# Kernel optimization log

Measured on AMD Instinct MI355X. Metric: run time of the kernel, lower is better.

Reference implementation:

```python
import jax, jax.numpy as jnp
import numpy as np

SR = 44100.0
BLOCK = 128
FC_MIN, FC_MAX = 2000.0, 20000.0
Q_MIN, Q_MAX = 0.1, 10.0


def setup_inputs() -> dict:
    key = jax.random.key(0)
    k1, k2 = jax.random.split(key)
    x = jax.random.normal(k1, (32, 1, 262144), dtype=jnp.float32)
    control_params = jax.random.uniform(k2, (32, 2, 262144), dtype=jnp.float32)
    return {"x": x, "control_params": control_params}


def _lowpass(x, control_params):
    B, _, S = x.shape
    nb = S // BLOCK  # S is a multiple of BLOCK, so no padding branch needed
    # AvgPool1d(kernel_size=BLOCK): one control value per block
    cp = control_params.reshape(B, 2, nb, BLOCK).mean(axis=-1)  # (B, 2, nb)
    # denormalize_parameters: linear map from [0,1] into (min, max)
    fc = cp[:, 0] * (FC_MAX - FC_MIN) + FC_MIN  # (B, nb)
    q = cp[:, 1] * (Q_MAX - Q_MIN) + Q_MIN      # (B, nb)
    # RBJ cookbook low-pass biquad coefficients, normalized by a0
    w0 = 2.0 * jnp.pi * fc / SR
    alpha = jnp.sin(w0) / (2.0 * q)
    cosw = jnp.cos(w0)
    a0 = 1.0 + alpha
    b0 = ((1.0 - cosw) * 0.5) / a0
    b1 = (1.0 - cosw) / a0
    b2 = b0
    a1 = (-2.0 * cosw) / a0
    a2 = (1.0 - alpha) / a0
    # Each block is filtered independently with zero initial state
    # (the torch loop calls sosfilt fresh per block) -> vectorize over B*nb lanes.
    xb = x.reshape(B, nb, BLOCK).reshape(B * nb, BLOCK)
    b0f, b1f, b2f = b0.reshape(-1), b1.reshape(-1), b2.reshape(-1)
    a1f, a2f = a1.reshape(-1), a2.reshape(-1)
    xt = xb.T  # (BLOCK, B*nb): scan over time within a block

    def step(carry, xn):
        # direct form II transposed biquad
        z1, z2 = carry
        y = b0f * xn + z1
        z1n = b1f * xn - a1f * y + z2
        z2n = b2f * xn - a2f * y
        return (z1n, z2n), y

    zeros = jnp.zeros((B * nb,), dtype=x.dtype)
    _, ys = jax.lax.scan(step, (zeros, zeros), xt)  # ys: (BLOCK, B*nb)
    out = ys.T.reshape(B, nb, BLOCK).reshape(B, 1, S)
    return out, fc, q


def reference(x, control_params):
    # returns (output, cutoff_freq_per_block, q_factor_per_block)
    return _lowpass(x, control_params)
```

## Files before the change

### kernel.cpp

```cpp
#include <hip/hip_runtime.h>
#include <math.h>

constexpr int   BATCH = 32;
constexpr int   S     = 262144;
constexpr int   BLK   = 128;
constexpr int   NB    = S / BLK;
constexpr float SRATE = 44100.0f;
constexpr float FC_MIN = 2000.0f, FC_MAX = 20000.0f;
constexpr float Q_MIN  = 0.1f,    Q_MAX  = 10.0f;

__global__ __launch_bounds__(256) void lowpass_kernel(
    const float* __restrict__ x,
    const float* __restrict__ cp,
    float* __restrict__ out,
    float* __restrict__ fc_out,
    float* __restrict__ q_out)
{
    const int tid = blockIdx.x * blockDim.x + threadIdx.x;
    const int b   = tid >> 11;
    const int blk = tid & (NB - 1);

    const float4* c0 = reinterpret_cast<const float4*>(
        cp + (size_t)b * 2 * S + (size_t)blk * BLK);
    const float4* c1 = c0 + S / 4;

    float s0 = 0.0f, s1 = 0.0f;
#pragma unroll 8
    for (int j = 0; j < BLK / 4; ++j) {
        float4 v = c0[j];
        s0 += (v.x + v.y) + (v.z + v.w);
    }
#pragma unroll 8
    for (int j = 0; j < BLK / 4; ++j) {
        float4 v = c1[j];
        s1 += (v.x + v.y) + (v.z + v.w);
    }
    const float m0 = s0 * (1.0f / BLK);
    const float m1 = s1 * (1.0f / BLK);

    const float fc = m0 * (FC_MAX - FC_MIN) + FC_MIN;
    const float q  = m1 * (Q_MAX - Q_MIN) + Q_MIN;

    const float w0 = 6.283185307179586f * fc / SRATE;
    float sw, cw;
    sincosf(w0, &sw, &cw);
    const float alpha = sw / (2.0f * q);
    const float a0inv = 1.0f / (1.0f + alpha);
    const float b0c = (1.0f - cw) * 0.5f * a0inv;
    const float b1c = (1.0f - cw) * a0inv;
    const float a1c = (-2.0f * cw) * a0inv;
    const float a2c = (1.0f - alpha) * a0inv;

    const float4* xp = reinterpret_cast<const float4*>(
        x + (size_t)b * S + (size_t)blk * BLK);
    float4* op = reinterpret_cast<float4*>(
        out + (size_t)b * S + (size_t)blk * BLK);

    float z1 = 0.0f, z2 = 0.0f;
#pragma unroll 8
    for (int j = 0; j < BLK / 4; ++j) {
        float4 xv = xp[j];
        float4 yv;

        {   float xn = xv.x;
            float y  = b0c * xn + z1;
            float z1n = b1c * xn - a1c * y + z2;
            z2 = b0c * xn - a2c * y;
            z1 = z1n;
            yv.x = y; }
        {   float xn = xv.y;
            float y  = b0c * xn + z1;
            float z1n = b1c * xn - a1c * y + z2;
            z2 = b0c * xn - a2c * y;
            z1 = z1n;
            yv.y = y; }
        {   float xn = xv.z;
            float y  = b0c * xn + z1;
            float z1n = b1c * xn - a1c * y + z2;
            z2 = b0c * xn - a2c * y;
            z1 = z1n;
            yv.z = y; }
        {   float xn = xv.w;
            float y  = b0c * xn + z1;
            float z1n = b1c * xn - a1c * y + z2;
            z2 = b0c * xn - a2c * y;
            z1 = z1n;
            yv.w = y; }

        op[j] = yv;
    }

    fc_out[tid] = fc;
    q_out[tid]  = q;
}

extern "C" void kernel_launch(void* const* d_in, const int* in_sizes, int n_in,
                              void* d_out, int out_size, void* d_ws, size_t ws_size,
                              hipStream_t stream) {
    const float* x  = (const float*)d_in[0];
    const float* cp = (const float*)d_in[1];

    float* out    = (float*)d_out;
    float* fc_out = out + (size_t)BATCH * S;
    float* q_out  = fc_out + (size_t)BATCH * NB;

    const int total = BATCH * NB;
    lowpass_kernel<<<total / 256, 256, 0, stream>>>(x, cp, out, fc_out, q_out);
}
```

Baseline: 29.83 us.

## Stage x tiles through LDS with coalesced loads and cooperative control averaging

```diff
diff --git a/kernel.cpp b/kernel.cpp
--- a/kernel.cpp
+++ b/kernel.cpp
@@ -9,89 +9,129 @@
 constexpr float FC_MIN = 2000.0f, FC_MAX = 20000.0f;
 constexpr float Q_MIN  = 0.1f,    Q_MAX  = 10.0f;
 
-__global__ __launch_bounds__(256) void lowpass_kernel(
+constexpr int WPB     = 64;
+constexpr int THREADS = 256;
+
+
+__global__ __launch_bounds__(THREADS) void lowpass_kernel(
     const float* __restrict__ x,
     const float* __restrict__ cp,
     float* __restrict__ out,
     float* __restrict__ fc_out,
     float* __restrict__ q_out)
 {
-    const int tid = blockIdx.x * blockDim.x + threadIdx.x;
-    const int b   = tid >> 11;
-    const int blk = tid & (NB - 1);
+    __shared__ float xs[WPB * BLK];
+    __shared__ float ms0[WPB], ms1[WPB];
 
-    const float4* c0 = reinterpret_cast<const float4*>(
-        cp + (size_t)b * 2 * S + (size_t)blk * BLK);
-    const float4* c1 = c0 + S / 4;
+    const int t    = threadIdx.x;
+    const int wg   = blockIdx.x;
+    const int b    = wg >> 5;
+    const int blk0 = (wg & 31) * WPB;
 
-    float s0 = 0.0f, s1 = 0.0f;
-#pragma unroll 8
-    for (int j = 0; j < BLK / 4; ++j) {
-        float4 v = c0[j];
-        s0 += (v.x + v.y) + (v.z + v.w);
-    }
-#pragma unroll 8
-    for (int j = 0; j < BLK / 4; ++j) {
-        float4 v = c1[j];
-        s1 += (v.x + v.y) + (v.z + v.w);
-    }
-    const float m0 = s0 * (1.0f / BLK);
-    const float m1 = s1 * (1.0f / BLK);
+    const size_t xbase = (size_t)b * S + (size_t)blk0 * BLK;
+    const float4* x4 = reinterpret_cast<const float4*>(x + xbase);
 
-    const float fc = m0 * (FC_MAX - FC_MIN) + FC_MIN;
-    const float q  = m1 * (Q_MAX - Q_MIN) + Q_MIN;
-
-    const float w0 = 6.283185307179586f * fc / SRATE;
-    float sw, cw;
-    sincosf(w0, &sw, &cw);
-    const float alpha = sw / (2.0f * q);
-    const float a0inv = 1.0f / (1.0f + alpha);
-    const float b0c = (1.0f - cw) * 0.5f * a0inv;
-    const float b1c = (1.0f - cw) * a0inv;
-    const float a1c = (-2.0f * cw) * a0inv;
-    const float a2c = (1.0f - alpha) * a0inv;
-
-    const float4* xp = reinterpret_cast<const float4*>(
-        x + (size_t)b * S + (size_t)blk * BLK);
-    float4* op = reinterpret_cast<float4*>(
-        out + (size_t)b * S + (size_t)blk * BLK);
-
-    float z1 = 0.0f, z2 = 0.0f;
-#pragma unroll 8
-    for (int j = 0; j < BLK / 4; ++j) {
-        float4 xv = xp[j];
-        float4 yv;
-
-        {   float xn = xv.x;
-            float y  = b0c * xn + z1;
-            float z1n = b1c * xn - a1c * y + z2;
-            z2 = b0c * xn - a2c * y;
-            z1 = z1n;
-            yv.x = y; }
-        {   float xn = xv.y;
-            float y  = b0c * xn + z1;
-            float z1n = b1c * xn - a1c * y + z2;
-            z2 = b0c * xn - a2c * y;
-            z1 = z1n;
-            yv.y = y; }
-        {   float xn = xv.z;
-            float y  = b0c * xn + z1;
-            float z1n = b1c * xn - a1c * y + z2;
-            z2 = b0c * xn - a2c * y;
-            z1 = z1n;
-            yv.z = y; }
-        {   float xn = xv.w;
-            float y  = b0c * xn + z1;
-            float z1n = b1c * xn - a1c * y + z2;
-            z2 = b0c * xn - a2c * y;
-            z1 = z1n;
-            yv.w = y; }
-
-        op[j] = yv;
+#pragma unroll
+    for (int k = 0; k < 8; ++k) {
+        const int D  = k * THREADS + t;
+        const int B  = D >> 5;
+        const int jp = D & 31;
+        const int src4 = B * 32 + (jp ^ (B & 7));
+        float* ldsb = xs + (size_t)(k * THREADS + (t & ~63)) * 4;
+        __builtin_amdgcn_global_load_lds(
+            (const __attribute__((address_space(1))) void*)(x4 + src4),
+            (__attribute__((address_space(3))) void*)ldsb,
+            16, 0, 0);
     }
 
-    fc_out[tid] = fc;
-    q_out[tid]  = q;
+    const size_t cpb = (size_t)b * 2 * S + (size_t)blk0 * BLK;
+    const float4* c0 = reinterpret_cast<const float4*>(cp + cpb);
+    const float4* c1 = reinterpret_cast<const float4*>(cp + cpb + S);
+
+    float4 v0[8], v1[8];
+#pragma unroll
+    for (int k = 0; k < 8; ++k) {
+        const int f = k * THREADS + t;
+        v0[k] = c0[f];
+        v1[k] = c1[f];
+    }
+#pragma unroll
+    for (int k = 0; k < 8; ++k) {
+        float s0 = (v0[k].x + v0[k].y) + (v0[k].z + v0[k].w);
+        float s1 = (v1[k].x + v1[k].y) + (v1[k].z + v1[k].w);
+#pragma unroll
+        for (int m = 1; m < 32; m <<= 1) {
+            s0 += __shfl_xor(s0, m);
+            s1 += __shfl_xor(s1, m);
+        }
+        if ((t & 31) == 0) {
+            const int B = k * 8 + (t >> 5);
+            ms0[B] = s0;
+            ms1[B] = s1;
+        }
+    }
+
+    __syncthreads();
+
+    if (t < WPB) {
+        const float m0 = ms0[t] * (1.0f / BLK);
+        const float m1 = ms1[t] * (1.0f / BLK);
+        const float fc = m0 * (FC_MAX - FC_MIN) + FC_MIN;
+        const float q  = m1 * (Q_MAX - Q_MIN) + Q_MIN;
+
+        const int gblk = b * NB + blk0 + t;
+        fc_out[gblk] = fc;
+        q_out[gblk]  = q;
+
+        const float w0 = 6.283185307179586f * fc / SRATE;
+        float sw, cw;
+        sincosf(w0, &sw, &cw);
+        const float alpha = sw / (2.0f * q);
+        const float a0inv = 1.0f / (1.0f + alpha);
+        const float b0c = (1.0f - cw) * 0.5f * a0inv;
+        const float b1c = (1.0f - cw) * a0inv;
+        const float a1c = (-2.0f * cw) * a0inv;
+        const float a2c = (1.0f - alpha) * a0inv;
+
+        float4* xs4 = reinterpret_cast<float4*>(xs);
+        const int swz = t & 7;
+        float z1 = 0.0f, z2 = 0.0f;
+#pragma unroll 8
+        for (int j = 0; j < 32; ++j) {
+            const int a = t * 32 + (j ^ swz);
+            float4 xv = xs4[a];
+            float4 yv;
+            {   float xn = xv.x;
+                float y   = b0c * xn + z1;
+                float z1n = b1c * xn - a1c * y + z2;
+                z2 = b0c * xn - a2c * y;  z1 = z1n;  yv.x = y; }
+            {   float xn = xv.y;
+                float y   = b0c * xn + z1;
+                float z1n = b1c * xn - a1c * y + z2;
+                z2 = b0c * xn - a2c * y;  z1 = z1n;  yv.y = y; }
+            {   float xn = xv.z;
+                float y   = b0c * xn + z1;
+                float z1n = b1c * xn - a1c * y + z2;
+                z2 = b0c * xn - a2c * y;  z1 = z1n;  yv.z = y; }
+            {   float xn = xv.w;
+                float y   = b0c * xn + z1;
+                float z1n = b1c * xn - a1c * y + z2;
+                z2 = b0c * xn - a2c * y;  z1 = z1n;  yv.w = y; }
+            xs4[a] = yv;
+        }
+    }
+
+    __syncthreads();
+
+    float4* o4 = reinterpret_cast<float4*>(out + xbase);
+    const float4* xs4 = reinterpret_cast<const float4*>(xs);
+#pragma unroll
+    for (int k = 0; k < 8; ++k) {
+        const int D  = k * THREADS + t;
+        const int B  = D >> 5;
+        const int jp = D & 31;
+        o4[B * 32 + (jp ^ (B & 7))] = xs4[D];
+    }
 }
 
 extern "C" void kernel_launch(void* const* d_in, const int* in_sizes, int n_in,
@@ -104,6 +144,7 @@
     float* fc_out = out + (size_t)BATCH * S;
     float* q_out  = fc_out + (size_t)BATCH * NB;
 
-    const int total = BATCH * NB;
-    lowpass_kernel<<<total / 256, 256, 0, stream>>>(x, cp, out, fc_out, q_out);
+    const int total_blocks = BATCH * NB;
+    const int grid = total_blocks / WPB;
+    lowpass_kernel<<<grid, THREADS, 0, stream>>>(x, cp, out, fc_out, q_out);
 }
```

Measured after the change: 27.72 us. -7.1%, faster.

## Stage x through swizzled LDS with async loads and cooperative coalesced control averaging

Applied to the files above, without the earlier changes.

```diff
diff --git a/kernel.cpp b/kernel.cpp
--- a/kernel.cpp
+++ b/kernel.cpp
@@ -9,89 +9,142 @@
 constexpr float FC_MIN = 2000.0f, FC_MAX = 20000.0f;
 constexpr float Q_MIN  = 0.1f,    Q_MAX  = 10.0f;
 
-__global__ __launch_bounds__(256) void lowpass_kernel(
+constexpr int WPB     = 32;
+constexpr int TILES   = 2;
+constexpr int THREADS = 256;
+constexpr int T_X4    = WPB * BLK / 4;
+
+typedef float f32x4 __attribute__((ext_vector_type(4)));
+
+#define GLOAD(dst, p)                                                     \
+  asm volatile("global_load_dwordx4 %0, %1, off"                          \
+               : "=v"(dst) : "v"(p) : "memory")
+
+#define PROCESS(U, VMSTR, R0, R1)                                          \
+  do {                                                                     \
+    asm volatile("s_waitcnt vmcnt(" VMSTR ")"                              \
+                 : "+v"(R0[0]), "+v"(R0[1]), "+v"(R0[2]), "+v"(R0[3]),     \
+                   "+v"(R1[0]), "+v"(R1[1]), "+v"(R1[2]), "+v"(R1[3]));    \
+    _Pragma("unroll")                                                      \
+    for (int k = 0; k < 4; ++k) {                                          \
+      float s0 = (R0[k].x + R0[k].y) + (R0[k].z + R0[k].w);                \
+      float s1 = (R1[k].x + R1[k].y) + (R1[k].z + R1[k].w);                \
+      s0 += __shfl_xor(s0, 1);  s1 += __shfl_xor(s1, 1);                   \
+      s0 += __shfl_xor(s0, 2);  s1 += __shfl_xor(s1, 2);                   \
+      s0 += __shfl_xor(s0, 4);  s1 += __shfl_xor(s1, 4);                   \
+      s0 += __shfl_xor(s0, 8);  s1 += __shfl_xor(s1, 8);                   \
+      s0 += __shfl_xor(s0, 16); s1 += __shfl_xor(s1, 16);                  \
+      if ((t & 31) == 0) {                                                 \
+        const int Bseg = k * 8 + (t >> 5);                                 \
+        ms0[U][Bseg] = s0;                                                 \
+        ms1[U][Bseg] = s1;                                                 \
+      }                                                                    \
+    }                                                                      \
+    asm volatile("s_waitcnt lgkmcnt(0)\n\ts_barrier" ::: "memory");        \
+    if (t < WPB) {                                                         \
+      const float m0 = ms0[U][t] * (1.0f / BLK);                           \
+      const float m1 = ms1[U][t] * (1.0f / BLK);                           \
+      const float fcv = m0 * (FC_MAX - FC_MIN) + FC_MIN;                   \
+      const float qv  = m1 * (Q_MAX - Q_MIN) + Q_MIN;                      \
+      const int gblk = b * NB + blk0 + (U) * WPB + t;                      \
+      fc_out[gblk] = fcv;                                                  \
+      q_out[gblk]  = qv;                                                   \
+      const float w0 = 6.283185307179586f * fcv / SRATE;                   \
+      float sw, cw;                                                        \
+      sincosf(w0, &sw, &cw);                                               \
+      const float alpha = sw / (2.0f * qv);                                \
+      const float a0inv = 1.0f / (1.0f + alpha);                           \
+      const float b0c = (1.0f - cw) * 0.5f * a0inv;          \
+      const float b1c = (1.0f - cw) * a0inv;                               \
+      const float a1c = (-2.0f * cw) * a0inv;                              \
+      const float a2c = (1.0f - alpha) * a0inv;                            \
+      f32x4* xs4u = reinterpret_cast<f32x4*>(xs[U]);                       \
+      const int swz = t & 7;                                               \
+      float z1 = 0.0f, z2 = 0.0f;                                          \
+      _Pragma("unroll 8")                                                  \
+      for (int j = 0; j < 32; ++j) {                                       \
+        const int a = t * 32 + (j ^ swz);                                  \
+        f32x4 xv = xs4u[a];                                                \
+        f32x4 yv;                                                          \
+        { float xn = xv.x; float y = b0c * xn + z1;                        \
+          float z1n = b1c * xn - a1c * y + z2;                             \
+          z2 = b0c * xn - a2c * y; z1 = z1n; yv.x = y; }                   \
+        { float xn = xv.y; float y = b0c * xn + z1;                        \
+          float z1n = b1c * xn - a1c * y + z2;                             \
+          z2 = b0c * xn - a2c * y; z1 = z1n; yv.y = y; }                   \
+        { float xn = xv.z; float y = b0c * xn + z1;                        \
+          float z1n = b1c * xn - a1c * y + z2;                             \
+          z2 = b0c * xn - a2c * y; z1 = z1n; yv.z = y; }                   \
+        { float xn = xv.w; float y = b0c * xn + z1;                        \
+          float z1n = b1c * xn - a1c * y + z2;                             \
+          z2 = b0c * xn - a2c * y; z1 = z1n; yv.w = y; }                   \
+        xs4u[a] = yv;                \
+      }                                                                    \
+    }                                                                      \
+    asm volatile("s_waitcnt lgkmcnt(0)\n\ts_barrier" ::: "memory");        \
+    {                                                                      \
+      f32x4* o4 = reinterpret_cast<f32x4*>(out + xbase);                   \
+      const f32x4* xs4u = reinterpret_cast<const f32x4*>(xs[U]);           \
+      _Pragma("unroll")                                                    \
+      for (int k = 0; k < 4; ++k) {                                        \
+        const int D  = k * THREADS + t;                                    \
+        const int Br = D >> 5;                                             \
+        const int jp = D & 31;                                             \
+        o4[(U) * T_X4 + Br * 32 + (jp ^ (Br & 7))] = xs4u[D];              \
+      }                                                                    \
+    }                                                                      \
+  } while (0)
+
+__global__ __launch_bounds__(THREADS) void lowpass_kernel(
     const float* __restrict__ x,
     const float* __restrict__ cp,
     float* __restrict__ out,
     float* __restrict__ fc_out,
     float* __restrict__ q_out)
 {
-    const int tid = blockIdx.x * blockDim.x + threadIdx.x;
-    const int b   = tid >> 11;
-    const int blk = tid & (NB - 1);
+    __shared__ float xs[TILES][WPB * BLK];
+    __shared__ float ms0[TILES][WPB], ms1[TILES][WPB];
 
-    const float4* c0 = reinterpret_cast<const float4*>(
-        cp + (size_t)b * 2 * S + (size_t)blk * BLK);
-    const float4* c1 = c0 + S / 4;
+    const int t    = threadIdx.x;
+    const int wg   = blockIdx.x;
+    const int b    = wg >> 5;
+    const int blk0 = (wg & 31) * (WPB * TILES);
 
-    float s0 = 0.0f, s1 = 0.0f;
-#pragma unroll 8
-    for (int j = 0; j < BLK / 4; ++j) {
-        float4 v = c0[j];
-        s0 += (v.x + v.y) + (v.z + v.w);
+    const size_t xbase = (size_t)b * S + (size_t)blk0 * BLK;
+    const f32x4* x4 = reinterpret_cast<const f32x4*>(x + xbase);
+    const f32x4* c0 = reinterpret_cast<const f32x4*>(
+        cp + (size_t)b * 2 * S + (size_t)blk0 * BLK);
+    const f32x4* c1 = c0 + S / 4;
+
+    f32x4 c0a[4], c1a[4], c0b[4], c1b[4];
+
+#pragma unroll
+    for (int k = 0; k < 4; ++k) {
+        const int D = k * THREADS + t, B = D >> 5, jp = D & 31;
+        __builtin_amdgcn_global_load_lds(
+            (const __attribute__((address_space(1))) void*)(x4 + (B * 32 + (jp ^ (B & 7)))),
+            (__attribute__((address_space(3))) void*)(&xs[0][(k * THREADS + (t & ~63)) * 4]),
+            16, 0, 0);
     }
-#pragma unroll 8
-    for (int j = 0; j < BLK / 4; ++j) {
-        float4 v = c1[j];
-        s1 += (v.x + v.y) + (v.z + v.w);
+#pragma unroll
+    for (int k = 0; k < 4; ++k) GLOAD(c0a[k], c0 + k * THREADS + t);
+#pragma unroll
+    for (int k = 0; k < 4; ++k) GLOAD(c1a[k], c1 + k * THREADS + t);
+#pragma unroll
+    for (int k = 0; k < 4; ++k) {
+        const int D = k * THREADS + t, B = D >> 5, jp = D & 31;
+        __builtin_amdgcn_global_load_lds(
+            (const __attribute__((address_space(1))) void*)(x4 + (T_X4 + B * 32 + (jp ^ (B & 7)))),
+            (__attribute__((address_space(3))) void*)(&xs[1][(k * THREADS + (t & ~63)) * 4]),
+            16, 0, 0);
     }
-    const float m0 = s0 * (1.0f / BLK);
-    const float m1 = s1 * (1.0f / BLK);
+#pragma unroll
+    for (int k = 0; k < 4; ++k) GLOAD(c0b[k], c0 + T_X4 + k * THREADS + t);
+#pragma unroll
+    for (int k = 0; k < 4; ++k) GLOAD(c1b[k], c1 + T_X4 + k * THREADS + t);
 
-    const float fc = m0 * (FC_MAX - FC_MIN) + FC_MIN;
-    const float q  = m1 * (Q_MAX - Q_MIN) + Q_MIN;
-
-    const float w0 = 6.283185307179586f * fc / SRATE;
-    float sw, cw;
-    sincosf(w0, &sw, &cw);
-    const float alpha = sw / (2.0f * q);
-    const float a0inv = 1.0f / (1.0f + alpha);
-    const float b0c = (1.0f - cw) * 0.5f * a0inv;
-    const float b1c = (1.0f - cw) * a0inv;
-    const float a1c = (-2.0f * cw) * a0inv;
-    const float a2c = (1.0f - alpha) * a0inv;
-
-    const float4* xp = reinterpret_cast<const float4*>(
-        x + (size_t)b * S + (size_t)blk * BLK);
-    float4* op = reinterpret_cast<float4*>(
-        out + (size_t)b * S + (size_t)blk * BLK);
-
-    float z1 = 0.0f, z2 = 0.0f;
-#pragma unroll 8
-    for (int j = 0; j < BLK / 4; ++j) {
-        float4 xv = xp[j];
-        float4 yv;
-
-        {   float xn = xv.x;
-            float y  = b0c * xn + z1;
-            float z1n = b1c * xn - a1c * y + z2;
-            z2 = b0c * xn - a2c * y;
-            z1 = z1n;
-            yv.x = y; }
-        {   float xn = xv.y;
-            float y  = b0c * xn + z1;
-            float z1n = b1c * xn - a1c * y + z2;
-            z2 = b0c * xn - a2c * y;
-            z1 = z1n;
-            yv.y = y; }
-        {   float xn = xv.z;
-            float y  = b0c * xn + z1;
-            float z1n = b1c * xn - a1c * y + z2;
-            z2 = b0c * xn - a2c * y;
-            z1 = z1n;
-            yv.z = y; }
-        {   float xn = xv.w;
-            float y  = b0c * xn + z1;
-            float z1n = b1c * xn - a1c * y + z2;
-            z2 = b0c * xn - a2c * y;
-            z1 = z1n;
-            yv.w = y; }
-
-        op[j] = yv;
-    }
-
-    fc_out[tid] = fc;
-    q_out[tid]  = q;
+    PROCESS(0, "12", c0a, c1a);
+    PROCESS(1, "4", c0b, c1b);
 }
 
 extern "C" void kernel_launch(void* const* d_in, const int* in_sizes, int n_in,
@@ -104,6 +157,7 @@
     float* fc_out = out + (size_t)BATCH * S;
     float* q_out  = fc_out + (size_t)BATCH * NB;
 
-    const int total = BATCH * NB;
-    lowpass_kernel<<<total / 256, 256, 0, stream>>>(x, cp, out, fc_out, q_out);
+    const int total_blocks = BATCH * NB;
+    const int grid = total_blocks / (WPB * TILES);
+    lowpass_kernel<<<grid, THREADS, 0, stream>>>(x, cp, out, fc_out, q_out);
 }
```

After: 30.89 us. 1.04x slower.

## Parallelize each block's biquad recurrence across 32 lanes with a matrix-power scan

Applied to the files above, without the earlier changes.

```diff
diff --git a/kernel.cpp b/kernel.cpp
--- a/kernel.cpp
+++ b/kernel.cpp
@@ -9,37 +9,44 @@
 constexpr float FC_MIN = 2000.0f, FC_MAX = 20000.0f;
 constexpr float Q_MIN  = 0.1f,    Q_MAX  = 10.0f;
 
-__global__ __launch_bounds__(256) void lowpass_kernel(
-    const float* __restrict__ x,
-    const float* __restrict__ cp,
-    float* __restrict__ out,
+
+__global__ __launch_bounds__(256) void lowpass_scan_kernel(
+    const float4* __restrict__ x4,
+    const float4* __restrict__ cp4,
+    float4* __restrict__ o4,
     float* __restrict__ fc_out,
     float* __restrict__ q_out)
 {
-    const int tid = blockIdx.x * blockDim.x + threadIdx.x;
-    const int b   = tid >> 11;
-    const int blk = tid & (NB - 1);
+    const int tid  = blockIdx.x * blockDim.x + threadIdx.x;
+    const int lane = tid & 63;
+    const int r    = lane & 31;
+    const int blkg = tid >> 5;
+    const int b    = blkg >> 11;
+    const int blkL = blkg & (NB - 1);
 
-    const float4* c0 = reinterpret_cast<const float4*>(
-        cp + (size_t)b * 2 * S + (size_t)blk * BLK);
-    const float4* c1 = c0 + S / 4;
+    const size_t xi  = (size_t)blkg * 32 + r;
+    const size_t c0i = (size_t)b * (2 * S / 4) + (size_t)blkL * 32 + r;
 
-    float s0 = 0.0f, s1 = 0.0f;
-#pragma unroll 8
-    for (int j = 0; j < BLK / 4; ++j) {
-        float4 v = c0[j];
-        s0 += (v.x + v.y) + (v.z + v.w);
-    }
-#pragma unroll 8
-    for (int j = 0; j < BLK / 4; ++j) {
-        float4 v = c1[j];
-        s1 += (v.x + v.y) + (v.z + v.w);
+    const float4 xv  = x4[xi];
+    const float4 c0v = cp4[c0i];
+    const float4 c1v = cp4[c0i + S / 4];
+
+    float s0 = (c0v.x + c0v.y) + (c0v.z + c0v.w);
+    float s1 = (c1v.x + c1v.y) + (c1v.z + c1v.w);
+#pragma unroll
+    for (int m = 1; m < 32; m <<= 1) {
+        s0 += __shfl_xor(s0, m);
+        s1 += __shfl_xor(s1, m);
     }
     const float m0 = s0 * (1.0f / BLK);
     const float m1 = s1 * (1.0f / BLK);
 
     const float fc = m0 * (FC_MAX - FC_MIN) + FC_MIN;
     const float q  = m1 * (Q_MAX - Q_MIN) + Q_MIN;
+    if (r == 0) {
+        fc_out[blkg] = fc;
+        q_out[blkg]  = q;
+    }
 
     const float w0 = 6.283185307179586f * fc / SRATE;
     float sw, cw;
@@ -50,60 +57,74 @@
     const float b1c = (1.0f - cw) * a0inv;
     const float a1c = (-2.0f * cw) * a0inv;
     const float a2c = (1.0f - alpha) * a0inv;
+    const float k1  = b1c - a1c * b0c;
+    const float k2  = b0c - a2c * b0c;
 
-    const float4* xp = reinterpret_cast<const float4*>(
-        x + (size_t)b * S + (size_t)blk * BLK);
-    float4* op = reinterpret_cast<float4*>(
-        out + (size_t)b * S + (size_t)blk * BLK);
-
-    float z1 = 0.0f, z2 = 0.0f;
-#pragma unroll 8
-    for (int j = 0; j < BLK / 4; ++j) {
-        float4 xv = xp[j];
-        float4 yv;
-
-        {   float xn = xv.x;
-            float y  = b0c * xn + z1;
-            float z1n = b1c * xn - a1c * y + z2;
-            z2 = b0c * xn - a2c * y;
-            z1 = z1n;
-            yv.x = y; }
-        {   float xn = xv.y;
-            float y  = b0c * xn + z1;
-            float z1n = b1c * xn - a1c * y + z2;
-            z2 = b0c * xn - a2c * y;
-            z1 = z1n;
-            yv.y = y; }
-        {   float xn = xv.z;
-            float y  = b0c * xn + z1;
-            float z1n = b1c * xn - a1c * y + z2;
-            z2 = b0c * xn - a2c * y;
-            z1 = z1n;
-            yv.z = y; }
-        {   float xn = xv.w;
-            float y  = b0c * xn + z1;
-            float z1n = b1c * xn - a1c * y + z2;
-            z2 = b0c * xn - a2c * y;
-            z1 = z1n;
-            yv.w = y; }
-
-        op[j] = yv;
+    float u1 = 0.0f, u2 = 0.0f;
+    {
+        float xn, t1;
+        xn = xv.x; t1 = u2 - a1c * u1 + k1 * xn; u2 = -a2c * u1 + k2 * xn; u1 = t1;
+        xn = xv.y; t1 = u2 - a1c * u1 + k1 * xn; u2 = -a2c * u1 + k2 * xn; u1 = t1;
+        xn = xv.z; t1 = u2 - a1c * u1 + k1 * xn; u2 = -a2c * u1 + k2 * xn; u1 = t1;
+        xn = xv.w; t1 = u2 - a1c * u1 + k1 * xn; u2 = -a2c * u1 + k2 * xn; u1 = t1;
     }
 
-    fc_out[tid] = fc;
-    q_out[tid]  = q;
+    float P00 = -a1c, P01 = 1.0f, P10 = -a2c, P11 = 0.0f;
+#define SQUARE_P()                                  \
+    {   float q00 = P00 * P00 + P01 * P10;          \
+        float q01 = P01 * (P00 + P11);              \
+        float q10 = P10 * (P00 + P11);              \
+        float q11 = P11 * P11 + P01 * P10;          \
+        P00 = q00; P01 = q01; P10 = q10; P11 = q11; }
+    SQUARE_P();
+    SQUARE_P();
+
+    float v1 = u1, v2 = u2;
+#define SCAN_STEP(d)                                        \
+    {   float w1 = __shfl_up(v1, d, 32);                    \
+        float w2 = __shfl_up(v2, d, 32);                    \
+        float t1 = v1 + P00 * w1 + P01 * w2;                \
+        float t2 = v2 + P10 * w1 + P11 * w2;                \
+        v1 = (r >= d) ? t1 : v1;                            \
+        v2 = (r >= d) ? t2 : v2; }
+    SCAN_STEP(1)  SQUARE_P();
+    SCAN_STEP(2)  SQUARE_P();
+    SCAN_STEP(4)  SQUARE_P();
+    SCAN_STEP(8)  SQUARE_P();
+    SCAN_STEP(16)
+#undef SCAN_STEP
+#undef SQUARE_P
+
+    float z1 = __shfl_up(v1, 1, 32);
+    float z2 = __shfl_up(v2, 1, 32);
+    if (r == 0) { z1 = 0.0f; z2 = 0.0f; }
+
+    float4 yv;
+    {
+        float xn, y, z1n;
+        xn = xv.x; y = b0c * xn + z1;
+        z1n = b1c * xn - a1c * y + z2; z2 = b0c * xn - a2c * y; z1 = z1n; yv.x = y;
+        xn = xv.y; y = b0c * xn + z1;
+        z1n = b1c * xn - a1c * y + z2; z2 = b0c * xn - a2c * y; z1 = z1n; yv.y = y;
+        xn = xv.z; y = b0c * xn + z1;
+        z1n = b1c * xn - a1c * y + z2; z2 = b0c * xn - a2c * y; z1 = z1n; yv.z = y;
+        xn = xv.w; y = b0c * xn + z1;
+        z1n = b1c * xn - a1c * y + z2; z2 = b0c * xn - a2c * y; z1 = z1n; yv.w = y;
+    }
+    o4[xi] = yv;
 }
 
 extern "C" void kernel_launch(void* const* d_in, const int* in_sizes, int n_in,
                               void* d_out, int out_size, void* d_ws, size_t ws_size,
                               hipStream_t stream) {
-    const float* x  = (const float*)d_in[0];
-    const float* cp = (const float*)d_in[1];
+    const float4* x4  = (const float4*)d_in[0];
+    const float4* cp4 = (const float4*)d_in[1];
 
     float* out    = (float*)d_out;
     float* fc_out = out + (size_t)BATCH * S;
     float* q_out  = fc_out + (size_t)BATCH * NB;
 
-    const int total = BATCH * NB;
-    lowpass_kernel<<<total / 256, 256, 0, stream>>>(x, cp, out, fc_out, q_out);
+    const int total_threads = BATCH * NB * 32;
+    lowpass_scan_kernel<<<total_threads / 256, 256, 0, stream>>>(
+        x4, cp4, (float4*)out, fc_out, q_out);
 }
```

Measured after the change: 25.68 us. 1.16x faster.
